# Kernel tuning notes

Hardware: AMD Instinct MI355X
Metric: run time of the kernel (lower is better)

## Reference

```python
import jax, jax.numpy as jnp
import numpy as np

RNN_SIZE = 1024
TSTEPS = 256
BATCH = 128


def setup_inputs() -> dict:
    key = jax.random.key(0)
    k1, k2, k3, k4, k5 = jax.random.split(key, 5)
    H = RNN_SIZE
    scale = 1.0 / np.sqrt(H)
    return {
        "cell_inputs": jax.random.normal(k1, (BATCH, H), dtype=jnp.float32),
        "hidden_states": jax.random.normal(k2, (BATCH, H), dtype=jnp.float32),
        # Keras GRUCell params (reset_after=True, default):
        "kernel": jax.random.normal(k3, (H, 3 * H), dtype=jnp.float32) * scale,
        "recurrent_kernel": jax.random.normal(k4, (H, 3 * H), dtype=jnp.float32) * scale,
        "bias": jax.random.normal(k5, (2, 3 * H), dtype=jnp.float32) * 0.01,
    }


def _gru_step(x, h, kernel, recurrent_kernel, bias):
    # Keras GRUCell math with reset_after=True (TF2 default).
    b_in, b_rec = bias[0], bias[1]
    mx = x @ kernel + b_in            # [B, 3H]
    mh = h @ recurrent_kernel + b_rec  # [B, 3H]
    xz, xr, xh = jnp.split(mx, 3, axis=-1)
    hz, hr, hh = jnp.split(mh, 3, axis=-1)
    z = jax.nn.sigmoid(xz + hz)
    r = jax.nn.sigmoid(xr + hr)
    h_cand = jnp.tanh(xh + r * hh)
    h_new = z * h + (1.0 - z) * h_cand
    return h_new  # GRUCell output == new state


def reference(cell_inputs, hidden_states, kernel, recurrent_kernel, bias):
    def step(carry, _):
        x, h = carry
        h_new = _gru_step(x, h, kernel, recurrent_kernel, bias)
        return (h_new, h_new), h_new

    (x_f, h_f), outs = jax.lax.scan(step, (cell_inputs, hidden_states), None, length=TSTEPS)
    outputs = jnp.transpose(outs, (1, 0, 2))  # [B, T, H]
    return outputs, h_f
```

## Files before the change

### kernel.cpp

```cpp
#include <hip/hip_runtime.h>
#include <hip/hip_bf16.h>

#define H 1024
#define B3H 3072
#define BATCH 128
#define TSTEPS 256
#define LROW 520
#define PLANE32 (32 * LROW)
#define NBLK 256
#define NTHR 768

typedef __attribute__((ext_vector_type(8))) short short8;
typedef __attribute__((ext_vector_type(4))) float f32x4;

static __device__ __forceinline__ float bf2f(__hip_bfloat16 v) { return __bfloat162float(v); }
static __device__ __forceinline__ unsigned short f2bf_bits(float f) {
    __hip_bfloat16 h = __float2bfloat16(f);
    return __builtin_bit_cast(unsigned short, h);
}
static __device__ __forceinline__ float bits2f(unsigned short b) {
    return bf2f(__builtin_bit_cast(__hip_bfloat16, b));
}
static __device__ __forceinline__ unsigned short bfbits(__hip_bfloat16 v) {
    return __builtin_bit_cast(unsigned short, v);
}
static __device__ __forceinline__ void split_bf(float v, unsigned short& hi, unsigned short& lo) {
    hi = f2bf_bits(v);
    lo = f2bf_bits(v - bits2f(hi));
}

#define BAR_OFF  128
#define PW_OFF   2048
#define PWL_OFF  (PW_OFF + 12582912)
#define XHI_OFF  (PWL_OFF + 12582912)
#define XLO_OFF  (XHI_OFF + 262144)
#define H0HI_OFF (XLO_OFF + 262144)
#define H0LO_OFF (H0HI_OFF + 262144)
#define H1HI_OFF (H0LO_OFF + 262144)
#define H1LO_OFF (H1HI_OFF + 262144)

__global__ void detect_dtype(const unsigned int* __restrict__ w, int* __restrict__ flag) {
    __shared__ int cnt[256];
    int c = 0;
    for (int i = threadIdx.x; i < 4096; i += 256) {
        unsigned int v = (w[i] >> 8) & 0x7f;
        c += (v >= 0x33 && v <= 0x3f) ? 1 : 0;
    }
    cnt[threadIdx.x] = c;
    __syncthreads();
    for (int s = 128; s > 0; s >>= 1) {
        if (threadIdx.x < s) cnt[threadIdx.x] += cnt[threadIdx.x + s];
        __syncthreads();
    }
    if (threadIdx.x == 0) *flag = (cnt[0] * 2 > 4096) ? 1 : 0;
}

__global__ void pack_w(const void* __restrict__ Kp, const void* __restrict__ Rp,
                       __hip_bfloat16* __restrict__ pwh, __hip_bfloat16* __restrict__ pwl,
                       const int* __restrict__ flag) {
    int idx = blockIdx.x * 256 + threadIdx.x;
    int lane = idx & 63;
    int kc   = (idx >> 6) & 31;
    int ns   = (idx >> 11) & 1;
    int it   = (idx >> 12) & 31;
    int g    = idx >> 17;
    if (g >= 6) return;
    const int isbf = *flag;
    int col   = (g % 3) * 1024 + it * 32 + ns * 16 + (lane & 15);
    int kbase = kc * 32 + (lane >> 4) * 8;
    unsigned short eh[8], el[8];
    if (isbf) {
        const __hip_bfloat16* src = (const __hip_bfloat16*)((g < 3) ? Kp : Rp);
#pragma unroll
        for (int j = 0; j < 8; ++j) { eh[j] = bfbits(src[(size_t)(kbase + j) * B3H + col]); el[j] = 0; }
    } else {
        const float* src = (const float*)((g < 3) ? Kp : Rp);
#pragma unroll
        for (int j = 0; j < 8; ++j) split_bf(src[(size_t)(kbase + j) * B3H + col], eh[j], el[j]);
    }
    uint4 vh, vl;
    vh.x = (unsigned int)eh[0] | ((unsigned int)eh[1] << 16);
    vh.y = (unsigned int)eh[2] | ((unsigned int)eh[3] << 16);
    vh.z = (unsigned int)eh[4] | ((unsigned int)eh[5] << 16);
    vh.w = (unsigned int)eh[6] | ((unsigned int)eh[7] << 16);
    vl.x = (unsigned int)el[0] | ((unsigned int)el[1] << 16);
    vl.y = (unsigned int)el[2] | ((unsigned int)el[3] << 16);
    vl.z = (unsigned int)el[4] | ((unsigned int)el[5] << 16);
    vl.w = (unsigned int)el[6] | ((unsigned int)el[7] << 16);
    *(uint4*)(pwh + (size_t)idx * 8) = vh;
    *(uint4*)(pwl + (size_t)idx * 8) = vl;
}

__global__ void init_bufs(const void* __restrict__ cin, const void* __restrict__ hs,
                          unsigned short* __restrict__ xhi, unsigned short* __restrict__ xlo,
                          unsigned short* __restrict__ hhi, unsigned short* __restrict__ hlo,
                          unsigned int* __restrict__ bar,
                          const int* __restrict__ flag) {
    int i = blockIdx.x * 256 + threadIdx.x;
    if (blockIdx.x == 0 && threadIdx.x < 480) bar[threadIdx.x] = 0;
    if (i >= BATCH * H) return;
    float xv, hv;
    if (*flag) {
        xv = bf2f(((const __hip_bfloat16*)cin)[i]);
        hv = bf2f(((const __hip_bfloat16*)hs)[i]);
    } else {
        xv = ((const float*)cin)[i];
        hv = ((const float*)hs)[i];
    }
    unsigned short a, b;
    split_bf(xv, a, b); xhi[i] = a; xlo[i] = b;
    split_bf(hv, a, b); hhi[i] = a; hlo[i] = b;
}

__launch_bounds__(NTHR, 1)
__global__ void gru_persistent(const unsigned short* __restrict__ xhi,
                               const unsigned short* __restrict__ xlo,
                               unsigned short* __restrict__ h0hi,
                               unsigned short* __restrict__ h0lo,
                               unsigned short* __restrict__ h1hi,
                               unsigned short* __restrict__ h1lo,
                               const __hip_bfloat16* __restrict__ pwh,
                               const __hip_bfloat16* __restrict__ pwl,
                               const void* __restrict__ bias,
                               void* __restrict__ out,
                               unsigned int* __restrict__ bar,
                               const int* __restrict__ flag) {
    __shared__ unsigned short sA[4 * PLANE32];
    __shared__ float sHold[512];
    __shared__ float sBias[96];

    const int tid  = threadIdx.x;
    const int w    = tid >> 6;
    const int g    = w >> 1;
    const int kh   = w & 1;
    const int lane = tid & 63;
    const int bt = blockIdx.x >> 6;
    const int it = blockIdx.x & 63;
    const int bbase = bt * 32;
    const int m0 = lane & 15;
    const int q  = lane >> 4;
    const int ibase0 = it * 16;
    const int isbf = *flag;

    {
        const __hip_bfloat16* bias_b = (const __hip_bfloat16*)bias;
        const float* bias_f = (const float*)bias;
        if (tid < 96) {
            int gg = tid >> 4;
            int i  = ibase0 + (tid & 15);
            int src = (gg < 3) ? (gg * 1024 + i) : (B3H + (gg - 3) * 1024 + i);
            sBias[tid] = isbf ? bf2f(bias_b[src]) : bias_f[src];
        }
    }

    const size_t boff = ((size_t)((g * 32 + (it >> 1)) * 2 + (it & 1)) * 32) * 64 + lane;
    const uint4* bh = (const uint4*)pwh + boff;
    const uint4* bl = (const uint4*)pwl + boff;

    __hip_bfloat16* outb = (__hip_bfloat16*)out;
    float* outf = (float*)out;

    for (int t = 0; t < TSTEPS; ++t) {
        const int cur = t & 1;
        const unsigned short* curhi = cur ? h1hi : h0hi;
        const unsigned short* curlo = cur ? h1lo : h0lo;
        unsigned short* dsthi = cur ? h0hi : h1hi;
        unsigned short* dstlo = cur ? h0lo : h1lo;

        f32x4 acc0 = {0.f, 0.f, 0.f, 0.f};
        f32x4 acc1 = {0.f, 0.f, 0.f, 0.f};

        if (t == 0) {
            for (int c = 0; c < 2; ++c) {
                if (c) __syncthreads();
                const int kstart = c * 512;
                for (int gi = tid; gi < 8192; gi += NTHR) {
                    int plane = gi >> 11;
                    int rem   = gi & 2047;
                    int row   = rem >> 6;
                    int kg    = rem & 63;
                    const unsigned short* src =
                        (plane == 0) ? xhi : (plane == 1) ? xlo : (plane == 2) ? curhi : curlo;
                    uint4 v = *(const uint4*)&src[(size_t)(bbase + row) * H + kstart + kg * 8];
                    *(uint4*)&sA[plane * PLANE32 + row * LROW + kg * 8] = v;
                }
                __syncthreads();
                if (kh == c) {
                    const unsigned short* aH0 = sA + ((g < 3) ? 0 : 2) * PLANE32;
                    const unsigned short* aL0 = aH0 + PLANE32;
#pragma unroll 4
                    for (int kc = 0; kc < 16; ++kc) {
                        const int kcg = c * 16 + kc;
                        short8 Bh = __builtin_bit_cast(short8, bh[(size_t)kcg * 64]);
                        short8 Bl = __builtin_bit_cast(short8, bl[(size_t)kcg * 64]);
                        const int koff = kc * 32 + q * 8;
                        short8 ah0 = *(const short8*)&aH0[m0 * LROW + koff];
                        short8 al0 = *(const short8*)&aL0[m0 * LROW + koff];
                        short8 ah1 = *(const short8*)&aH0[(16 + m0) * LROW + koff];
                        short8 al1 = *(const short8*)&aL0[(16 + m0) * LROW + koff];
                        acc0 = __builtin_amdgcn_mfma_f32_16x16x32_bf16(ah0, Bh, acc0, 0, 0, 0);
                        acc0 = __builtin_amdgcn_mfma_f32_16x16x32_bf16(ah0, Bl, acc0, 0, 0, 0);
                        acc0 = __builtin_amdgcn_mfma_f32_16x16x32_bf16(al0, Bh, acc0, 0, 0, 0);
                        acc1 = __builtin_amdgcn_mfma_f32_16x16x32_bf16(ah1, Bh, acc1, 0, 0, 0);
                        acc1 = __builtin_amdgcn_mfma_f32_16x16x32_bf16(ah1, Bl, acc1, 0, 0, 0);
                        acc1 = __builtin_amdgcn_mfma_f32_16x16x32_bf16(al1, Bh, acc1, 0, 0, 0);
                    }
                }
            }
        } else {
            const unsigned short* gp[11];
            int ld[11];
#pragma unroll
            for (int r2 = 0; r2 < 11; ++r2) {
                int gi = r2 * NTHR + tid;
                if (gi >= 8192) gi -= 8192;
                int plane = gi >> 11;
                int rem   = gi & 2047;
                int row   = rem >> 6;
                int kg    = rem & 63;
                const unsigned short* src = (plane & 1) ? curlo : curhi;
                gp[r2] = &src[(size_t)(bbase + row) * H + (plane >> 1) * 512 + kg * 8];
                ld[r2] = plane * PLANE32 + row * LROW + kg * 8;
            }
            uint4 v0, v1, v2, v3, v4, v5, v6, v7, v8, v9, v10;
            asm volatile(
                "global_load_dwordx4 %0, %11, off sc0 sc1\n\t"
                "global_load_dwordx4 %1, %12, off sc0 sc1\n\t"
                "global_load_dwordx4 %2, %13, off sc0 sc1\n\t"
                "global_load_dwordx4 %3, %14, off sc0 sc1\n\t"
                "global_load_dwordx4 %4, %15, off sc0 sc1\n\t"
                "global_load_dwordx4 %5, %16, off sc0 sc1\n\t"
                "global_load_dwordx4 %6, %17, off sc0 sc1\n\t"
                "global_load_dwordx4 %7, %18, off sc0 sc1\n\t"
                "global_load_dwordx4 %8, %19, off sc0 sc1\n\t"
                "global_load_dwordx4 %9, %20, off sc0 sc1\n\t"
                "global_load_dwordx4 %10, %21, off sc0 sc1\n\t"
                "s_waitcnt vmcnt(0)"
                : "=&v"(v0), "=&v"(v1), "=&v"(v2), "=&v"(v3), "=&v"(v4), "=&v"(v5),
                  "=&v"(v6), "=&v"(v7), "=&v"(v8), "=&v"(v9), "=&v"(v10)
                : "v"(gp[0]), "v"(gp[1]), "v"(gp[2]), "v"(gp[3]), "v"(gp[4]), "v"(gp[5]),
                  "v"(gp[6]), "v"(gp[7]), "v"(gp[8]), "v"(gp[9]), "v"(gp[10])
                : "memory");
            *(uint4*)&sA[ld[0]]  = v0;
            *(uint4*)&sA[ld[1]]  = v1;
            *(uint4*)&sA[ld[2]]  = v2;
            *(uint4*)&sA[ld[3]]  = v3;
            *(uint4*)&sA[ld[4]]  = v4;
            *(uint4*)&sA[ld[5]]  = v5;
            *(uint4*)&sA[ld[6]]  = v6;
            *(uint4*)&sA[ld[7]]  = v7;
            *(uint4*)&sA[ld[8]]  = v8;
            *(uint4*)&sA[ld[9]]  = v9;
            *(uint4*)&sA[ld[10]] = v10;
            __syncthreads();

            uint4 wph[4], wpl[4];
#pragma unroll
            for (int p = 0; p < 4; ++p) {
                wph[p] = bh[(size_t)(kh * 16 + p) * 64];
                wpl[p] = bl[(size_t)(kh * 16 + p) * 64];
            }
            const int aBase = kh * 2 * PLANE32;
#pragma unroll
            for (int kc = 0; kc < 16; ++kc) {
                const int s = kc & 3;
                short8 Bh = __builtin_bit_cast(short8, wph[s]);
                short8 Bl = __builtin_bit_cast(short8, wpl[s]);
                if (kc + 4 < 16) {
                    wph[s] = bh[(size_t)(kh * 16 + kc + 4) * 64];
                    wpl[s] = bl[(size_t)(kh * 16 + kc + 4) * 64];
                }
                const int koff = kc * 32 + q * 8;
                short8 ah0 = *(const short8*)&sA[aBase + m0 * LROW + koff];
                short8 al0 = *(const short8*)&sA[aBase + PLANE32 + m0 * LROW + koff];
                short8 ah1 = *(const short8*)&sA[aBase + (16 + m0) * LROW + koff];
                short8 al1 = *(const short8*)&sA[aBase + PLANE32 + (16 + m0) * LROW + koff];
                acc0 = __builtin_amdgcn_mfma_f32_16x16x32_bf16(ah0, Bh, acc0, 0, 0, 0);
                acc0 = __builtin_amdgcn_mfma_f32_16x16x32_bf16(ah0, Bl, acc0, 0, 0, 0);
                acc0 = __builtin_amdgcn_mfma_f32_16x16x32_bf16(al0, Bh, acc0, 0, 0, 0);
                acc1 = __builtin_amdgcn_mfma_f32_16x16x32_bf16(ah1, Bh, acc1, 0, 0, 0);
                acc1 = __builtin_amdgcn_mfma_f32_16x16x32_bf16(ah1, Bl, acc1, 0, 0, 0);
                acc1 = __builtin_amdgcn_mfma_f32_16x16x32_bf16(al1, Bh, acc1, 0, 0, 0);
            }
        }

        __syncthreads();
        float* sG = (float*)sA;
        {
#pragma unroll
            for (int r = 0; r < 4; ++r) {
                int mrow = q * 4 + r;
                sG[((g * 2 + kh) * 2 + 0) * 256 + mrow * 16 + m0] = acc0[r];
                sG[((g * 2 + kh) * 2 + 1) * 256 + mrow * 16 + m0] = acc1[r];
            }
        }
        __syncthreads();

        if (tid < 256) {
            const int e0   = tid * 2;
            const int mloc = e0 >> 4;
            const int nl0  = e0 & 15;
            const int mt   = mloc >> 4;
            const int rt   = mloc & 15;
            const int b    = bbase + mloc;
            const int i0   = ibase0 + nl0;
            const size_t hidx0 = (size_t)b * H + i0;
            float hn[2];
            unsigned short nh[2], nl[2];
#pragma unroll
            for (int j = 0; j < 2; ++j) {
                const int nloc = nl0 + j;
                const int base = rt * 16 + nloc;
                float xz = sG[(0 * 4 + mt) * 256 + base] + sG[(0 * 4 + 2 + mt) * 256 + base];
                float xr = sG[(1 * 4 + mt) * 256 + base] + sG[(1 * 4 + 2 + mt) * 256 + base];
                float xh = sG[(2 * 4 + mt) * 256 + base] + sG[(2 * 4 + 2 + mt) * 256 + base];
                float hz = sG[(3 * 4 + mt) * 256 + base] + sG[(3 * 4 + 2 + mt) * 256 + base];
                float hr = sG[(4 * 4 + mt) * 256 + base] + sG[(4 * 4 + 2 + mt) * 256 + base];
                float hh = sG[(5 * 4 + mt) * 256 + base] + sG[(5 * 4 + 2 + mt) * 256 + base];
                float zlin = xz + sBias[nloc]      + hz + sBias[48 + nloc];
                float rlin = xr + sBias[16 + nloc] + hr + sBias[64 + nloc];
                float xht  = xh + sBias[32 + nloc];
                float hht  = hh + sBias[80 + nloc];
                float z  = 1.0f / (1.0f + expf(-zlin));
                float r  = 1.0f / (1.0f + expf(-rlin));
                float hc = tanhf(xht + r * hht);
                const int e = e0 + j;
                float hold = t ? sHold[e]
                               : (bits2f(curhi[hidx0 + j]) + bits2f(curlo[hidx0 + j]));
                float hnew = z * hold + (1.0f - z) * hc;
                sHold[e] = hnew;
                hn[j] = hnew;
                split_bf(hnew, nh[j], nl[j]);
            }
            if (t < TSTEPS - 1) {
                unsigned int hiw = (unsigned int)nh[0] | ((unsigned int)nh[1] << 16);
                unsigned int low = (unsigned int)nl[0] | ((unsigned int)nl[1] << 16);
                __hip_atomic_store((unsigned int*)&dsthi[hidx0], hiw,
                                   __ATOMIC_RELAXED, __HIP_MEMORY_SCOPE_AGENT);
                __hip_atomic_store((unsigned int*)&dstlo[hidx0], low,
                                   __ATOMIC_RELAXED, __HIP_MEMORY_SCOPE_AGENT);
            }
            const size_t o1 = (size_t)b * (TSTEPS * H) + (size_t)t * H + i0;
            if (isbf) {
                outb[o1]     = __float2bfloat16(hn[0]);
                outb[o1 + 1] = __float2bfloat16(hn[1]);
                if (t == TSTEPS - 1) {
                    outb[(size_t)BATCH * TSTEPS * H + hidx0]     = __float2bfloat16(hn[0]);
                    outb[(size_t)BATCH * TSTEPS * H + hidx0 + 1] = __float2bfloat16(hn[1]);
                }
            } else {
                outf[o1]     = hn[0];
                outf[o1 + 1] = hn[1];
                if (t == TSTEPS - 1) {
                    outf[(size_t)BATCH * TSTEPS * H + hidx0]     = hn[0];
                    outf[(size_t)BATCH * TSTEPS * H + hidx0 + 1] = hn[1];
                }
            }
        }

        if (t < TSTEPS - 1) {
            asm volatile("s_waitcnt vmcnt(0)" ::: "memory");
            __syncthreads();
            if (tid == 0) {
                __hip_atomic_store(&bar[bt * 64 + it], (unsigned int)(t + 1),
                                   __ATOMIC_RELAXED, __HIP_MEMORY_SCOPE_AGENT);
            }
            if (w == 0) {
                const unsigned int target = (unsigned int)(t + 1);
                for (;;) {
                    unsigned int v = __hip_atomic_load(&bar[bt * 64 + lane],
                                        __ATOMIC_RELAXED, __HIP_MEMORY_SCOPE_AGENT);
                    if (__all(v >= target)) break;
                    __builtin_amdgcn_s_sleep(1);
                }
            }
            __syncthreads();
        }
    }
}

extern "C" void kernel_launch(void* const* d_in, const int* in_sizes, int n_in,
                              void* d_out, int out_size, void* d_ws, size_t ws_size,
                              hipStream_t stream) {
    const void* cin  = d_in[0];
    const void* hs   = d_in[1];
    const void* Kw   = d_in[2];
    const void* Rw   = d_in[3];
    const void* bias = d_in[4];

    char* ws = (char*)d_ws;
    int* flag = (int*)ws;
    unsigned int* bar = (unsigned int*)(ws + BAR_OFF);
    __hip_bfloat16* pwh = (__hip_bfloat16*)(ws + PW_OFF);
    __hip_bfloat16* pwl = (__hip_bfloat16*)(ws + PWL_OFF);
    unsigned short* xhi  = (unsigned short*)(ws + XHI_OFF);
    unsigned short* xlo  = (unsigned short*)(ws + XLO_OFF);
    unsigned short* h0hi = (unsigned short*)(ws + H0HI_OFF);
    unsigned short* h0lo = (unsigned short*)(ws + H0LO_OFF);
    unsigned short* h1hi = (unsigned short*)(ws + H1HI_OFF);
    unsigned short* h1lo = (unsigned short*)(ws + H1LO_OFF);

    detect_dtype<<<1, 256, 0, stream>>>((const unsigned int*)Kw, flag);
    pack_w<<<3072, 256, 0, stream>>>(Kw, Rw, pwh, pwl, flag);
    init_bufs<<<512, 256, 0, stream>>>(cin, hs, xhi, xlo, h0hi, h0lo, bar, flag);

    const unsigned short* xhi_c = xhi;
    const unsigned short* xlo_c = xlo;
    const __hip_bfloat16* pwh_c = pwh;
    const __hip_bfloat16* pwl_c = pwl;
    const int* flag_c = flag;
    void* kargs[] = {
        (void*)&xhi_c, (void*)&xlo_c,
        (void*)&h0hi, (void*)&h0lo, (void*)&h1hi, (void*)&h1lo,
        (void*)&pwh_c, (void*)&pwl_c,
        (void*)&bias, (void*)&d_out, (void*)&bar, (void*)&flag_c
    };
    hipLaunchCooperativeKernel((void*)gru_persistent, dim3(256), dim3(NTHR),
                               kargs, 0, stream);
}
```

Before: 3.911 ms.

## Assign two gate tiles per wave with K split in quarters to reuse A fragments

Warps are remapped so that each handles two adjacent gate column tiles (a pair of gates) over a quarter of K, instead of one gate over half of K. In steady-state steps the A fragments read from LDS are then shared by both gate tiles, which halves LDS A traffic per MFMA. Weight prefetch for the first four k-chunks is issued before the hidden-state global loads, so it overlaps with them. The cost is a four-way partial-sum reduction in the epilogue, which uses a padded row stride of 18 to reduce bank conflicts, and more registers per wave.

```diff
diff --git a/kernel.cpp b/kernel.cpp
--- a/kernel.cpp
+++ b/kernel.cpp
@@ -131,8 +131,10 @@
 
     const int tid  = threadIdx.x;
     const int w    = tid >> 6;
-    const int g    = w >> 1;
-    const int kh   = w & 1;
+    const int ctp  = w >> 2;
+    const int kq   = w & 3;
+    const int ga   = 2 * ctp;
+    const int gb   = 2 * ctp + 1;
     const int lane = tid & 63;
     const int bt = blockIdx.x >> 6;
     const int it = blockIdx.x & 63;
@@ -153,9 +155,14 @@
         }
     }
 
-    const size_t boff = ((size_t)((g * 32 + (it >> 1)) * 2 + (it & 1)) * 32) * 64 + lane;
-    const uint4* bh = (const uint4*)pwh + boff;
-    const uint4* bl = (const uint4*)pwl + boff;
+    const int it2 = it >> 1, ns = it & 1;
+    const size_t boffA = ((size_t)((ga * 32 + it2) * 2 + ns) * 32) * 64 + lane;
+    const size_t boffB = ((size_t)((gb * 32 + it2) * 2 + ns) * 32) * 64 + lane;
+    const uint4* bhA = (const uint4*)pwh + boffA;
+    const uint4* blA = (const uint4*)pwl + boffA;
+    const uint4* bhB = (const uint4*)pwh + boffB;
+    const uint4* blB = (const uint4*)pwl + boffB;
+    const int kcg0 = kq * 8;
 
     __hip_bfloat16* outb = (__hip_bfloat16*)out;
     float* outf = (float*)out;
@@ -167,13 +174,14 @@
         unsigned short* dsthi = cur ? h0hi : h1hi;
         unsigned short* dstlo = cur ? h0lo : h1lo;
 
-        f32x4 acc0 = {0.f, 0.f, 0.f, 0.f};
-        f32x4 acc1 = {0.f, 0.f, 0.f, 0.f};
+        f32x4 acc_a0 = {0.f, 0.f, 0.f, 0.f};
+        f32x4 acc_a1 = {0.f, 0.f, 0.f, 0.f};
+        f32x4 acc_b0 = {0.f, 0.f, 0.f, 0.f};
+        f32x4 acc_b1 = {0.f, 0.f, 0.f, 0.f};
 
         if (t == 0) {
             for (int c = 0; c < 2; ++c) {
                 if (c) __syncthreads();
-                const int kstart = c * 512;
                 for (int gi = tid; gi < 8192; gi += NTHR) {
                     int plane = gi >> 11;
                     int rem   = gi & 2047;
@@ -181,33 +189,54 @@
                     int kg    = rem & 63;
                     const unsigned short* src =
                         (plane == 0) ? xhi : (plane == 1) ? xlo : (plane == 2) ? curhi : curlo;
-                    uint4 v = *(const uint4*)&src[(size_t)(bbase + row) * H + kstart + kg * 8];
+                    uint4 v = *(const uint4*)&src[(size_t)(bbase + row) * H + c * 512 + kg * 8];
                     *(uint4*)&sA[plane * PLANE32 + row * LROW + kg * 8] = v;
                 }
                 __syncthreads();
-                if (kh == c) {
-                    const unsigned short* aH0 = sA + ((g < 3) ? 0 : 2) * PLANE32;
-                    const unsigned short* aL0 = aH0 + PLANE32;
-#pragma unroll 4
-                    for (int kc = 0; kc < 16; ++kc) {
-                        const int kcg = c * 16 + kc;
-                        short8 Bh = __builtin_bit_cast(short8, bh[(size_t)kcg * 64]);
-                        short8 Bl = __builtin_bit_cast(short8, bl[(size_t)kcg * 64]);
-                        const int koff = kc * 32 + q * 8;
-                        short8 ah0 = *(const short8*)&aH0[m0 * LROW + koff];
-                        short8 al0 = *(const short8*)&aL0[m0 * LROW + koff];
-                        short8 ah1 = *(const short8*)&aH0[(16 + m0) * LROW + koff];
-                        short8 al1 = *(const short8*)&aL0[(16 + m0) * LROW + koff];
-                        acc0 = __builtin_amdgcn_mfma_f32_16x16x32_bf16(ah0, Bh, acc0, 0, 0, 0);
-                        acc0 = __builtin_amdgcn_mfma_f32_16x16x32_bf16(ah0, Bl, acc0, 0, 0, 0);
-                        acc0 = __builtin_amdgcn_mfma_f32_16x16x32_bf16(al0, Bh, acc0, 0, 0, 0);
-                        acc1 = __builtin_amdgcn_mfma_f32_16x16x32_bf16(ah1, Bh, acc1, 0, 0, 0);
-                        acc1 = __builtin_amdgcn_mfma_f32_16x16x32_bf16(ah1, Bl, acc1, 0, 0, 0);
-                        acc1 = __builtin_amdgcn_mfma_f32_16x16x32_bf16(al1, Bh, acc1, 0, 0, 0);
+                if ((kq >> 1) == c) {
+                    const int baseA_ = (ga < 3) ? 0 : 2 * PLANE32;
+                    const int baseB_ = (gb < 3) ? 0 : 2 * PLANE32;
+#pragma unroll 2
+                    for (int kc = 0; kc < 8; ++kc) {
+                        const int kcg = kcg0 + kc;
+                        short8 Bha = __builtin_bit_cast(short8, bhA[(size_t)kcg * 64]);
+                        short8 Bla = __builtin_bit_cast(short8, blA[(size_t)kcg * 64]);
+                        short8 Bhb = __builtin_bit_cast(short8, bhB[(size_t)kcg * 64]);
+                        short8 Blb = __builtin_bit_cast(short8, blB[(size_t)kcg * 64]);
+                        const int koff = ((kq & 1) * 8 + kc) * 32 + q * 8;
+                        short8 aha0 = *(const short8*)&sA[baseA_ + m0 * LROW + koff];
+                        short8 ala0 = *(const short8*)&sA[baseA_ + PLANE32 + m0 * LROW + koff];
+                        short8 aha1 = *(const short8*)&sA[baseA_ + (16 + m0) * LROW + koff];
+                        short8 ala1 = *(const short8*)&sA[baseA_ + PLANE32 + (16 + m0) * LROW + koff];
+                        short8 ahb0 = *(const short8*)&sA[baseB_ + m0 * LROW + koff];
+                        short8 alb0 = *(const short8*)&sA[baseB_ + PLANE32 + m0 * LROW + koff];
+                        short8 ahb1 = *(const short8*)&sA[baseB_ + (16 + m0) * LROW + koff];
+                        short8 alb1 = *(const short8*)&sA[baseB_ + PLANE32 + (16 + m0) * LROW + koff];
+                        acc_a0 = __builtin_amdgcn_mfma_f32_16x16x32_bf16(aha0, Bha, acc_a0, 0, 0, 0);
+                        acc_a0 = __builtin_amdgcn_mfma_f32_16x16x32_bf16(aha0, Bla, acc_a0, 0, 0, 0);
+                        acc_a0 = __builtin_amdgcn_mfma_f32_16x16x32_bf16(ala0, Bha, acc_a0, 0, 0, 0);
+                        acc_a1 = __builtin_amdgcn_mfma_f32_16x16x32_bf16(aha1, Bha, acc_a1, 0, 0, 0);
+                        acc_a1 = __builtin_amdgcn_mfma_f32_16x16x32_bf16(aha1, Bla, acc_a1, 0, 0, 0);
+                        acc_a1 = __builtin_amdgcn_mfma_f32_16x16x32_bf16(ala1, Bha, acc_a1, 0, 0, 0);
+                        acc_b0 = __builtin_amdgcn_mfma_f32_16x16x32_bf16(ahb0, Bhb, acc_b0, 0, 0, 0);
+                        acc_b0 = __builtin_amdgcn_mfma_f32_16x16x32_bf16(ahb0, Blb, acc_b0, 0, 0, 0);
+                        acc_b0 = __builtin_amdgcn_mfma_f32_16x16x32_bf16(alb0, Bhb, acc_b0, 0, 0, 0);
+                        acc_b1 = __builtin_amdgcn_mfma_f32_16x16x32_bf16(ahb1, Bhb, acc_b1, 0, 0, 0);
+                        acc_b1 = __builtin_amdgcn_mfma_f32_16x16x32_bf16(ahb1, Blb, acc_b1, 0, 0, 0);
+                        acc_b1 = __builtin_amdgcn_mfma_f32_16x16x32_bf16(alb1, Bhb, acc_b1, 0, 0, 0);
                     }
                 }
             }
         } else {
+            uint4 phA[4], plA[4], phB[4], plB[4];
+#pragma unroll
+            for (int p = 0; p < 4; ++p) {
+                phA[p] = bhA[(size_t)(kcg0 + p) * 64];
+                plA[p] = blA[(size_t)(kcg0 + p) * 64];
+                phB[p] = bhB[(size_t)(kcg0 + p) * 64];
+                plB[p] = blB[(size_t)(kcg0 + p) * 64];
+            }
+
             const unsigned short* gp[11];
             int ld[11];
 #pragma unroll
@@ -254,33 +283,38 @@
             *(uint4*)&sA[ld[10]] = v10;
             __syncthreads();
 
-            uint4 wph[4], wpl[4];
-#pragma unroll
-            for (int p = 0; p < 4; ++p) {
-                wph[p] = bh[(size_t)(kh * 16 + p) * 64];
-                wpl[p] = bl[(size_t)(kh * 16 + p) * 64];
-            }
-            const int aBase = kh * 2 * PLANE32;
-#pragma unroll
-            for (int kc = 0; kc < 16; ++kc) {
+#pragma unroll
+            for (int kc = 0; kc < 8; ++kc) {
+                const int kcg = kcg0 + kc;
                 const int s = kc & 3;
-                short8 Bh = __builtin_bit_cast(short8, wph[s]);
-                short8 Bl = __builtin_bit_cast(short8, wpl[s]);
-                if (kc + 4 < 16) {
-                    wph[s] = bh[(size_t)(kh * 16 + kc + 4) * 64];
-                    wpl[s] = bl[(size_t)(kh * 16 + kc + 4) * 64];
-                }
-                const int koff = kc * 32 + q * 8;
-                short8 ah0 = *(const short8*)&sA[aBase + m0 * LROW + koff];
-                short8 al0 = *(const short8*)&sA[aBase + PLANE32 + m0 * LROW + koff];
-                short8 ah1 = *(const short8*)&sA[aBase + (16 + m0) * LROW + koff];
-                short8 al1 = *(const short8*)&sA[aBase + PLANE32 + (16 + m0) * LROW + koff];
-                acc0 = __builtin_amdgcn_mfma_f32_16x16x32_bf16(ah0, Bh, acc0, 0, 0, 0);
-                acc0 = __builtin_amdgcn_mfma_f32_16x16x32_bf16(ah0, Bl, acc0, 0, 0, 0);
-                acc0 = __builtin_amdgcn_mfma_f32_16x16x32_bf16(al0, Bh, acc0, 0, 0, 0);
-                acc1 = __builtin_amdgcn_mfma_f32_16x16x32_bf16(ah1, Bh, acc1, 0, 0, 0);
-                acc1 = __builtin_amdgcn_mfma_f32_16x16x32_bf16(ah1, Bl, acc1, 0, 0, 0);
-                acc1 = __builtin_amdgcn_mfma_f32_16x16x32_bf16(al1, Bh, acc1, 0, 0, 0);
+                short8 Bha = __builtin_bit_cast(short8, phA[s]);
+                short8 Bla = __builtin_bit_cast(short8, plA[s]);
+                short8 Bhb = __builtin_bit_cast(short8, phB[s]);
+                short8 Blb = __builtin_bit_cast(short8, plB[s]);
+                if (kc + 4 < 8) {
+                    phA[s] = bhA[(size_t)(kcg + 4) * 64];
+                    plA[s] = blA[(size_t)(kcg + 4) * 64];
+                    phB[s] = bhB[(size_t)(kcg + 4) * 64];
+                    plB[s] = blB[(size_t)(kcg + 4) * 64];
+                }
+                const int base = (kcg >> 4) * 2 * PLANE32;
+                const int koff = (kcg & 15) * 32 + q * 8;
+                short8 ah0 = *(const short8*)&sA[base + m0 * LROW + koff];
+                short8 al0 = *(const short8*)&sA[base + PLANE32 + m0 * LROW + koff];
+                short8 ah1 = *(const short8*)&sA[base + (16 + m0) * LROW + koff];
+                short8 al1 = *(const short8*)&sA[base + PLANE32 + (16 + m0) * LROW + koff];
+                acc_a0 = __builtin_amdgcn_mfma_f32_16x16x32_bf16(ah0, Bha, acc_a0, 0, 0, 0);
+                acc_a0 = __builtin_amdgcn_mfma_f32_16x16x32_bf16(ah0, Bla, acc_a0, 0, 0, 0);
+                acc_a0 = __builtin_amdgcn_mfma_f32_16x16x32_bf16(al0, Bha, acc_a0, 0, 0, 0);
+                acc_a1 = __builtin_amdgcn_mfma_f32_16x16x32_bf16(ah1, Bha, acc_a1, 0, 0, 0);
+                acc_a1 = __builtin_amdgcn_mfma_f32_16x16x32_bf16(ah1, Bla, acc_a1, 0, 0, 0);
+                acc_a1 = __builtin_amdgcn_mfma_f32_16x16x32_bf16(al1, Bha, acc_a1, 0, 0, 0);
+                acc_b0 = __builtin_amdgcn_mfma_f32_16x16x32_bf16(ah0, Bhb, acc_b0, 0, 0, 0);
+                acc_b0 = __builtin_amdgcn_mfma_f32_16x16x32_bf16(ah0, Blb, acc_b0, 0, 0, 0);
+                acc_b0 = __builtin_amdgcn_mfma_f32_16x16x32_bf16(al0, Bhb, acc_b0, 0, 0, 0);
+                acc_b1 = __builtin_amdgcn_mfma_f32_16x16x32_bf16(ah1, Bhb, acc_b1, 0, 0, 0);
+                acc_b1 = __builtin_amdgcn_mfma_f32_16x16x32_bf16(ah1, Blb, acc_b1, 0, 0, 0);
+                acc_b1 = __builtin_amdgcn_mfma_f32_16x16x32_bf16(al1, Bhb, acc_b1, 0, 0, 0);
             }
         }
 
@@ -289,9 +323,11 @@
         {
 #pragma unroll
             for (int r = 0; r < 4; ++r) {
-                int mrow = q * 4 + r;
-                sG[((g * 2 + kh) * 2 + 0) * 256 + mrow * 16 + m0] = acc0[r];
-                sG[((g * 2 + kh) * 2 + 1) * 256 + mrow * 16 + m0] = acc1[r];
+                int row = q * 4 + r;
+                sG[((ga * 4 + kq) * 2 + 0) * 288 + row * 18 + m0] = acc_a0[r];
+                sG[((ga * 4 + kq) * 2 + 1) * 288 + row * 18 + m0] = acc_a1[r];
+                sG[((gb * 4 + kq) * 2 + 0) * 288 + row * 18 + m0] = acc_b0[r];
+                sG[((gb * 4 + kq) * 2 + 1) * 288 + row * 18 + m0] = acc_b1[r];
             }
         }
         __syncthreads();
@@ -300,8 +336,8 @@
             const int e0   = tid * 2;
             const int mloc = e0 >> 4;
             const int nl0  = e0 & 15;
-            const int mt   = mloc >> 4;
-            const int rt   = mloc & 15;
+            const int rt   = mloc >> 4;
+            const int rr   = mloc & 15;
             const int b    = bbase + mloc;
             const int i0   = ibase0 + nl0;
             const size_t hidx0 = (size_t)b * H + i0;
@@ -309,18 +345,17 @@
             unsigned short nh[2], nl[2];
 #pragma unroll
             for (int j = 0; j < 2; ++j) {
-                const int nloc = nl0 + j;
-                const int base = rt * 16 + nloc;
-                float xz = sG[(0 * 4 + mt) * 256 + base] + sG[(0 * 4 + 2 + mt) * 256 + base];
-                float xr = sG[(1 * 4 + mt) * 256 + base] + sG[(1 * 4 + 2 + mt) * 256 + base];
-                float xh = sG[(2 * 4 + mt) * 256 + base] + sG[(2 * 4 + 2 + mt) * 256 + base];
-                float hz = sG[(3 * 4 + mt) * 256 + base] + sG[(3 * 4 + 2 + mt) * 256 + base];
-                float hr = sG[(4 * 4 + mt) * 256 + base] + sG[(4 * 4 + 2 + mt) * 256 + base];
-                float hh = sG[(5 * 4 + mt) * 256 + base] + sG[(5 * 4 + 2 + mt) * 256 + base];
-                float zlin = xz + sBias[nloc]      + hz + sBias[48 + nloc];
-                float rlin = xr + sBias[16 + nloc] + hr + sBias[64 + nloc];
-                float xht  = xh + sBias[32 + nloc];
-                float hht  = hh + sBias[80 + nloc];
+                const int c = nl0 + j;
+                const int rbase = rr * 18 + c;
+#define GV(g) (sG[(((g) * 4 + 0) * 2 + rt) * 288 + rbase] + sG[(((g) * 4 + 1) * 2 + rt) * 288 + rbase] \
+             + sG[(((g) * 4 + 2) * 2 + rt) * 288 + rbase] + sG[(((g) * 4 + 3) * 2 + rt) * 288 + rbase])
+                float xz = GV(0), xr = GV(1), xh = GV(2);
+                float hz = GV(3), hr = GV(4), hh = GV(5);
+#undef GV
+                float zlin = xz + sBias[c]      + hz + sBias[48 + c];
+                float rlin = xr + sBias[16 + c] + hr + sBias[64 + c];
+                float xht  = xh + sBias[32 + c];
+                float hht  = hh + sBias[80 + c];
                 float z  = 1.0f / (1.0f + expf(-zlin));
                 float r  = 1.0f / (1.0f + expf(-rlin));
                 float hc = tanhf(xht + r * hht);
```

After: 5.655 ms. 1.45x slower.
